# Optimization experiments

Measured on AMD Instinct MI355X. Metric: run time of the kernel, lower is better.

The kernel has to match this reference:

```python
import jax, jax.numpy as jnp
import numpy as np

NEG = -1000000.0  # mask value used by the original module


def setup_inputs() -> dict:
    key = jax.random.key(0)
    ks = jax.random.split(key, 8)
    N, D_IN, D_Q, D_K, E = 8192, 512, 512, 512, 262144
    s = 1.0 / np.sqrt(D_IN)
    return {
        "x": jax.random.normal(ks[0], (N, D_IN), dtype=jnp.float32),
        "edge_index": jax.random.randint(ks[1], (2, E), 0, N, dtype=jnp.int64),
        "Wq": jax.random.normal(ks[2], (D_IN, D_Q), dtype=jnp.float32) * s,
        "bq": jax.random.normal(ks[3], (D_Q,), dtype=jnp.float32) * 0.01,
        "Wk": jax.random.normal(ks[4], (D_IN, D_K), dtype=jnp.float32) * s,
        "bk": jax.random.normal(ks[5], (D_K,), dtype=jnp.float32) * 0.01,
        "Wv": jax.random.normal(ks[6], (D_IN, D_K), dtype=jnp.float32) * s,
        "bv": jax.random.normal(ks[7], (D_K,), dtype=jnp.float32) * 0.01,
    }


def reference(x, edge_index, Wq, bq, Wk, bk, Wv, bv):
    # Linear projections (x: [N, D_in])
    q = x @ Wq + bq  # [N, Dq]
    k = x @ Wk + bk  # [N, Dk]
    v = x @ Wv + bv  # [N, Dk]

    N = x.shape[0]
    # Dense adjacency from edge list (matches torch scatter adjacency[e0, e1] = 1)
    adj = jnp.zeros((N, N), dtype=x.dtype).at[edge_index[0], edge_index[1]].set(1.0)

    # Full scores (ptr=None branch), scaled by sqrt(Dq)
    a = (q @ k.T) / jnp.sqrt(jnp.asarray(q.shape[-1], dtype=x.dtype))
    a = a * adj + (1.0 - adj) * NEG

    attn = jax.nn.softmax(a, axis=-1)  # [N, N]
    return attn @ v  # [N, Dk]
```

## Files before the change

### kernel.cpp

```cpp
#include <hip/hip_runtime.h>


#define N_NODES 8192
#define DIM 512
#define MASK_WORDS 256
#define CAPW 512

typedef __attribute__((ext_vector_type(8))) short short8;
typedef __attribute__((ext_vector_type(4))) float f32x4;

__device__ __forceinline__ unsigned short f2bf(float f) {
    unsigned int u = __float_as_uint(f);
    u += 0x7fffu + ((u >> 16) & 1u);
    return (unsigned short)(u >> 16);
}
__device__ __forceinline__ float bf_lo(unsigned int w) { return __uint_as_float(w << 16); }
__device__ __forceinline__ float bf_hi(unsigned int w) { return __uint_as_float(w & 0xffff0000u); }

__device__ __forceinline__ float wred_sum(float s) {
    #pragma unroll
    for (int off = 1; off <= 32; off <<= 1) s += __shfl_xor(s, off, 64);
    return s;
}
__device__ __forceinline__ float wred_max(float s) {
    #pragma unroll
    for (int off = 1; off <= 32; off <<= 1) s = fmaxf(s, __shfl_xor(s, off, 64));
    return s;
}
__device__ __forceinline__ int wred_sumi(int s) {
    #pragma unroll
    for (int off = 1; off <= 32; off <<= 1) s += __shfl_xor(s, off, 64);
    return s;
}
__device__ __forceinline__ float dot8(uint4 a, uint4 b) {
    return bf_lo(a.x) * bf_lo(b.x) + bf_hi(a.x) * bf_hi(b.x)
         + bf_lo(a.y) * bf_lo(b.y) + bf_hi(a.y) * bf_hi(b.y)
         + bf_lo(a.z) * bf_lo(b.z) + bf_hi(a.z) * bf_hi(b.z)
         + bf_lo(a.w) * bf_lo(b.w) + bf_hi(a.w) * bf_hi(b.w);
}

__global__ __launch_bounds__(256) void prep(
    const float* __restrict__ x, unsigned short* __restrict__ xb,
    const float* __restrict__ Wq, const float* __restrict__ Wk,
    const float* __restrict__ Wv, unsigned short* __restrict__ Wt,
    const int* __restrict__ ei, unsigned int* __restrict__ mask, int E)
{
    __shared__ float sm[32][33];
    const int b = blockIdx.x;
    if (b < 4096) {
        int i = b * 256 + threadIdx.x;
        float4 f = ((const float4*)x)[i];
        ushort4 o;
        o.x = f2bf(f.x); o.y = f2bf(f.y); o.z = f2bf(f.z); o.w = f2bf(f.w);
        ((ushort4*)xb)[i] = o;
    } else if (b < 4864) {
        int bb = b - 4096;
        int which = bb >> 8, t = bb & 255;
        const float* __restrict__ W = (which == 0) ? Wq : (which == 1) ? Wk : Wv;
        unsigned short* __restrict__ outp = Wt + (size_t)which * DIM * DIM;
        int n0 = (t & 15) * 32, k0 = (t >> 4) * 32;
        int tx = threadIdx.x & 31, ty = threadIdx.x >> 5;
        #pragma unroll
        for (int r = 0; r < 4; ++r)
            sm[ty + 8 * r][tx] = W[(size_t)(k0 + ty + 8 * r) * DIM + n0 + tx];
        __syncthreads();
        #pragma unroll
        for (int r = 0; r < 4; ++r)
            outp[(size_t)(n0 + ty + 8 * r) * DIM + k0 + tx] = f2bf(sm[tx][ty + 8 * r]);
    } else {
        int e = (b - 4864) * 256 + threadIdx.x;
        if (e < E) {
            int src = ei[e];
            int dst = ei[E + e];
            atomicOr(&mask[(size_t)src * MASK_WORDS + (dst >> 5)], 1u << (dst & 31));
        }
    }
}

__device__ __forceinline__ void load_lds16(const unsigned short* g, unsigned short* l) {
    __builtin_amdgcn_global_load_lds(
        (const __attribute__((address_space(1))) unsigned int*)g,
        (__attribute__((address_space(3))) unsigned int*)l, 16, 0, 0);
}

__global__ __launch_bounds__(256) void mfma_gemm(
    const unsigned short* __restrict__ xb, const unsigned short* __restrict__ Wt,
    const float* __restrict__ bq, const float* __restrict__ bk, const float* __restrict__ bv,
    unsigned short* __restrict__ q, unsigned short* __restrict__ k, unsigned short* __restrict__ v)
{
    const int which = blockIdx.z;
    const unsigned short* __restrict__ Bm = Wt + (size_t)which * DIM * DIM;
    const float* __restrict__ bias = (which == 0) ? bq : (which == 1) ? bk : bv;
    unsigned short* __restrict__ outp = (which == 0) ? q : (which == 1) ? k : v;

    const int row0 = blockIdx.y * 128;
    const int col0 = blockIdx.x * 128;
    const int tid = threadIdx.x;
    const int lane = tid & 63;
    const int w = tid >> 6;
    const int wm = (w >> 1) * 64;
    const int wn = (w & 1) * 64;
    const int L = lane & 15;
    const int quad = lane >> 4;

    __shared__ unsigned short As[128 * 32];
    __shared__ unsigned short Bs[128 * 32];

    f32x4 zero = {0.f, 0.f, 0.f, 0.f};
    f32x4 acc[4][4];
    #pragma unroll
    for (int i = 0; i < 4; ++i)
        #pragma unroll
        for (int j = 0; j < 4; ++j) acc[i][j] = zero;

    const int m0 = tid >> 2;
    const int ko = (tid & 3) << 3;

    for (int k0 = 0; k0 < DIM; k0 += 32) {
        load_lds16(xb + (size_t)(row0 + m0) * DIM + k0 + ko,      As + tid * 8);
        load_lds16(xb + (size_t)(row0 + 64 + m0) * DIM + k0 + ko, As + 2048 + tid * 8);
        load_lds16(Bm + (size_t)(col0 + m0) * DIM + k0 + ko,      Bs + tid * 8);
        load_lds16(Bm + (size_t)(col0 + 64 + m0) * DIM + k0 + ko, Bs + 2048 + tid * 8);
        __syncthreads();

        short8 a[4], bfr[4];
        #pragma unroll
        for (int i = 0; i < 4; ++i)
            a[i] = *(const short8*)(const void*)&As[(wm + i * 16 + L) * 32 + quad * 8];
        #pragma unroll
        for (int j = 0; j < 4; ++j)
            bfr[j] = *(const short8*)(const void*)&Bs[(wn + j * 16 + L) * 32 + quad * 8];

        #pragma unroll
        for (int i = 0; i < 4; ++i)
            #pragma unroll
            for (int j = 0; j < 4; ++j)
                acc[i][j] = __builtin_amdgcn_mfma_f32_16x16x32_bf16(a[i], bfr[j], acc[i][j], 0, 0, 0);
        __syncthreads();
    }

    float biasv[4];
    #pragma unroll
    for (int j = 0; j < 4; ++j) biasv[j] = bias[col0 + wn + j * 16 + L];
    #pragma unroll
    for (int i = 0; i < 4; ++i) {
        int r0 = row0 + wm + i * 16 + quad * 4;
        #pragma unroll
        for (int j = 0; j < 4; ++j) {
            int c = col0 + wn + j * 16 + L;
            #pragma unroll
            for (int r = 0; r < 4; ++r)
                outp[(size_t)(r0 + r) * DIM + c] = f2bf(acc[i][j][r] + biasv[j]);
        }
    }
}

__global__ __launch_bounds__(256) void attn_kernel(
    const unsigned short* __restrict__ q, const unsigned short* __restrict__ k,
    const unsigned short* __restrict__ v, const unsigned int* __restrict__ mask,
    float* __restrict__ out)
{
    __shared__ unsigned short nbr[4][CAPW];
    __shared__ float pw[4][CAPW];
    __shared__ int cnt[4];

    const int tid = threadIdx.x;
    const int lane = tid & 63;
    const int wid = tid >> 6;
    const int row = blockIdx.x * 4 + wid;

    const uint4 qv = *(const uint4*)(q + (size_t)row * DIM + lane * 8);
    const unsigned int* __restrict__ mrow = mask + (size_t)row * MASK_WORDS;

    int pc = 0;
    #pragma unroll
    for (int t = 0; t < 4; ++t) pc += __popc(mrow[lane + 64 * t]);
    const int total = wred_sumi(pc);

    float o[8];
    #pragma unroll
    for (int i = 0; i < 8; ++i) o[i] = 0.f;

    if (total == 0) {
        for (int j = 0; j < N_NODES; ++j) {
            uint4 vv = *(const uint4*)(v + (size_t)j * DIM + lane * 8);
            o[0] += bf_lo(vv.x); o[1] += bf_hi(vv.x);
            o[2] += bf_lo(vv.y); o[3] += bf_hi(vv.y);
            o[4] += bf_lo(vv.z); o[5] += bf_hi(vv.z);
            o[6] += bf_lo(vv.w); o[7] += bf_hi(vv.w);
        }
        float4 r0 = {o[0], o[1], o[2], o[3]};
        float4 r1 = {o[4], o[5], o[6], o[7]};
        const float s = 1.0f / N_NODES;
        r0.x *= s; r0.y *= s; r0.z *= s; r0.w *= s;
        r1.x *= s; r1.y *= s; r1.z *= s; r1.w *= s;
        *(float4*)(out + (size_t)row * DIM + lane * 8) = r0;
        *(float4*)(out + (size_t)row * DIM + lane * 8 + 4) = r1;
        return;
    }

    const int nchunks = (total <= CAPW) ? 1 : 16;
    const int wpc = (nchunks == 1) ? MASK_WORDS : 16;
    const float scale = 0.044194173824159220f;

    float m_run = -3.0e38f, l_run = 0.f;

    for (int c = 0; c < nchunks; ++c) {
        if (lane == 0) cnt[wid] = 0;
        for (int wi = lane; wi < wpc; wi += 64) {
            unsigned int ww = mrow[c * wpc + wi];
            while (ww) {
                int bpos = __ffs(ww) - 1; ww &= ww - 1;
                int pos = atomicAdd(&cnt[wid], 1);
                nbr[wid][pos] = (unsigned short)((c * wpc + wi) * 32 + bpos);
            }
        }
        const int cn = cnt[wid];
        if (cn == 0) continue;

        for (int p = 0; p < cn; p += 2) {
            int j0 = nbr[wid][p];
            int j1 = nbr[wid][(p + 1 < cn) ? p + 1 : p];
            uint4 k0v = *(const uint4*)(k + (size_t)j0 * DIM + lane * 8);
            uint4 k1v = *(const uint4*)(k + (size_t)j1 * DIM + lane * 8);
            float s0 = wred_sum(dot8(qv, k0v));
            float s1 = wred_sum(dot8(qv, k1v));
            if (lane == 0) {
                pw[wid][p] = s0 * scale;
                if (p + 1 < cn) pw[wid][p + 1] = s1 * scale;
            }
        }

        float mc = -3.0e38f;
        for (int p = lane; p < cn; p += 64) mc = fmaxf(mc, pw[wid][p]);
        mc = wred_max(mc);
        const float mnew = fmaxf(m_run, mc);
        const float f = __expf(m_run - mnew);
        float ls = 0.f;
        for (int p = lane; p < cn; p += 64) {
            float e = __expf(pw[wid][p] - mnew);
            pw[wid][p] = e;
            ls += e;
        }
        l_run = l_run * f + wred_sum(ls);
        m_run = mnew;
        #pragma unroll
        for (int i = 0; i < 8; ++i) o[i] *= f;

        int p = 0;
        for (; p + 2 <= cn; p += 2) {
            int j0 = nbr[wid][p], j1 = nbr[wid][p + 1];
            float w0 = pw[wid][p], w1 = pw[wid][p + 1];
            uint4 v0 = *(const uint4*)(v + (size_t)j0 * DIM + lane * 8);
            uint4 v1 = *(const uint4*)(v + (size_t)j1 * DIM + lane * 8);
            o[0] += w0 * bf_lo(v0.x) + w1 * bf_lo(v1.x);
            o[1] += w0 * bf_hi(v0.x) + w1 * bf_hi(v1.x);
            o[2] += w0 * bf_lo(v0.y) + w1 * bf_lo(v1.y);
            o[3] += w0 * bf_hi(v0.y) + w1 * bf_hi(v1.y);
            o[4] += w0 * bf_lo(v0.z) + w1 * bf_lo(v1.z);
            o[5] += w0 * bf_hi(v0.z) + w1 * bf_hi(v1.z);
            o[6] += w0 * bf_lo(v0.w) + w1 * bf_lo(v1.w);
            o[7] += w0 * bf_hi(v0.w) + w1 * bf_hi(v1.w);
        }
        if (p < cn) {
            int j0 = nbr[wid][p];
            float w0 = pw[wid][p];
            uint4 v0 = *(const uint4*)(v + (size_t)j0 * DIM + lane * 8);
            o[0] += w0 * bf_lo(v0.x); o[1] += w0 * bf_hi(v0.x);
            o[2] += w0 * bf_lo(v0.y); o[3] += w0 * bf_hi(v0.y);
            o[4] += w0 * bf_lo(v0.z); o[5] += w0 * bf_hi(v0.z);
            o[6] += w0 * bf_lo(v0.w); o[7] += w0 * bf_hi(v0.w);
        }
    }

    const float inv = 1.0f / l_run;
    float4 r0 = {o[0] * inv, o[1] * inv, o[2] * inv, o[3] * inv};
    float4 r1 = {o[4] * inv, o[5] * inv, o[6] * inv, o[7] * inv};
    *(float4*)(out + (size_t)row * DIM + lane * 8) = r0;
    *(float4*)(out + (size_t)row * DIM + lane * 8 + 4) = r1;
}

extern "C" void kernel_launch(void* const* d_in, const int* in_sizes, int n_in,
                              void* d_out, int out_size, void* d_ws, size_t ws_size,
                              hipStream_t stream)
{
    const float* x  = (const float*)d_in[0];
    const int*   ei = (const int*)d_in[1];
    const float* Wq = (const float*)d_in[2];
    const float* bq = (const float*)d_in[3];
    const float* Wk = (const float*)d_in[4];
    const float* bk = (const float*)d_in[5];
    const float* Wv = (const float*)d_in[6];
    const float* bv = (const float*)d_in[7];
    float* out = (float*)d_out;

    const int E = in_sizes[1] / 2;
    const size_t NM = (size_t)N_NODES * DIM;

    unsigned short* xb = (unsigned short*)d_ws;
    unsigned short* Wt = xb + NM;
    unsigned short* qb = Wt + (size_t)3 * DIM * DIM;
    unsigned short* kb = qb + NM;
    unsigned short* vb = kb + NM;
    unsigned int* mask = (unsigned int*)(vb + NM);

    hipMemsetAsync(mask, 0, (size_t)N_NODES * MASK_WORDS * sizeof(unsigned int), stream);

    prep<<<4864 + (E + 255) / 256, 256, 0, stream>>>(x, xb, Wq, Wk, Wv, Wt, ei, mask, E);

    mfma_gemm<<<dim3(DIM / 128, N_NODES / 128, 3), 256, 0, stream>>>(
        xb, Wt, bq, bk, bv, qb, kb, vb);

    attn_kernel<<<N_NODES / 4, 256, 0, stream>>>(qb, kb, vb, mask, out);
}
```

Baseline: 173.1 us.

## Split each attention row across four waves, fuse mask clear, remap GEMM tiles by XCD

The attention kernel now gives each row a whole block. Each of the four waves handles a quarter of the neighbour mask, keeps its own online softmax, and the partial results are merged through LDS, with gathers unrolled by four. The mask memset moves into the bf16 conversion kernel and the edge scatter becomes its own launch. GEMM tiles are remapped so row blocks group per XCD for L2 locality. This aims to shorten per-row serial latency and improve occupancy, at the cost of extra block syncs, LDS traffic and one more launch.

```diff
diff --git a/kernel.cpp b/kernel.cpp
--- a/kernel.cpp
+++ b/kernel.cpp
@@ -4,7 +4,7 @@
 #define N_NODES 8192
 #define DIM 512
 #define MASK_WORDS 256
-#define CAPW 512
+#define SCAP 256
 
 typedef __attribute__((ext_vector_type(8))) short short8;
 typedef __attribute__((ext_vector_type(4))) float f32x4;
@@ -39,11 +39,11 @@
          + bf_lo(a.w) * bf_lo(b.w) + bf_hi(a.w) * bf_hi(b.w);
 }
 
-__global__ __launch_bounds__(256) void prep(
+__global__ __launch_bounds__(256) void prep1(
     const float* __restrict__ x, unsigned short* __restrict__ xb,
     const float* __restrict__ Wq, const float* __restrict__ Wk,
     const float* __restrict__ Wv, unsigned short* __restrict__ Wt,
-    const int* __restrict__ ei, unsigned int* __restrict__ mask, int E)
+    unsigned int* __restrict__ mask)
 {
     __shared__ float sm[32][33];
     const int b = blockIdx.x;
@@ -53,7 +53,8 @@
         ushort4 o;
         o.x = f2bf(f.x); o.y = f2bf(f.y); o.z = f2bf(f.z); o.w = f2bf(f.w);
         ((ushort4*)xb)[i] = o;
-    } else if (b < 4864) {
+        ((uint2*)mask)[i] = make_uint2(0u, 0u);
+    } else {
         int bb = b - 4096;
         int which = bb >> 8, t = bb & 255;
         const float* __restrict__ W = (which == 0) ? Wq : (which == 1) ? Wk : Wv;
@@ -67,14 +68,17 @@
         #pragma unroll
         for (int r = 0; r < 4; ++r)
             outp[(size_t)(n0 + ty + 8 * r) * DIM + k0 + tx] = f2bf(sm[tx][ty + 8 * r]);
-    } else {
-        int e = (b - 4864) * 256 + threadIdx.x;
-        if (e < E) {
-            int src = ei[e];
-            int dst = ei[E + e];
-            atomicOr(&mask[(size_t)src * MASK_WORDS + (dst >> 5)], 1u << (dst & 31));
-        }
-    }
+    }
+}
+
+__global__ __launch_bounds__(256) void prep2(
+    const int* __restrict__ ei, unsigned int* __restrict__ mask, int E)
+{
+    int e = blockIdx.x * 256 + threadIdx.x;
+    if (e >= E) return;
+    int src = ei[e];
+    int dst = ei[E + e];
+    atomicOr(&mask[(size_t)src * MASK_WORDS + (dst >> 5)], 1u << (dst & 31));
 }
 
 __device__ __forceinline__ void load_lds16(const unsigned short* g, unsigned short* l) {
@@ -86,15 +90,21 @@
 __global__ __launch_bounds__(256) void mfma_gemm(
     const unsigned short* __restrict__ xb, const unsigned short* __restrict__ Wt,
     const float* __restrict__ bq, const float* __restrict__ bk, const float* __restrict__ bv,
-    unsigned short* __restrict__ q, unsigned short* __restrict__ k, unsigned short* __restrict__ v)
-{
-    const int which = blockIdx.z;
+    unsigned short* __restrict__ qkv)
+{
+    const int p = blockIdx.x;
+    const int xcd = p & 7;
+    const int s = p >> 3;
+    const int mloc = s / 12;
+    const int n = s - 12 * mloc;
+    const int which = n >> 2;
+    const int row0 = (xcd * 8 + mloc) << 7;
+    const int col0 = (n & 3) << 7;
+
     const unsigned short* __restrict__ Bm = Wt + (size_t)which * DIM * DIM;
     const float* __restrict__ bias = (which == 0) ? bq : (which == 1) ? bk : bv;
-    unsigned short* __restrict__ outp = (which == 0) ? q : (which == 1) ? k : v;
-
-    const int row0 = blockIdx.y * 128;
-    const int col0 = blockIdx.x * 128;
+    unsigned short* __restrict__ outp = qkv + (size_t)which * N_NODES * DIM;
+
     const int tid = threadIdx.x;
     const int lane = tid & 63;
     const int w = tid >> 6;
@@ -160,74 +170,85 @@
     const unsigned short* __restrict__ v, const unsigned int* __restrict__ mask,
     float* __restrict__ out)
 {
-    __shared__ unsigned short nbr[4][CAPW];
-    __shared__ float pw[4][CAPW];
+    __shared__ unsigned short nbr[4][SCAP];
+    __shared__ float pw[4][SCAP];
+    __shared__ float buf[4][DIM];
+    __shared__ float sm_m[4], sm_l[4];
+    __shared__ int degs[4];
     __shared__ int cnt[4];
 
     const int tid = threadIdx.x;
     const int lane = tid & 63;
     const int wid = tid >> 6;
-    const int row = blockIdx.x * 4 + wid;
+    const int row = blockIdx.x;
 
     const uint4 qv = *(const uint4*)(q + (size_t)row * DIM + lane * 8);
-    const unsigned int* __restrict__ mrow = mask + (size_t)row * MASK_WORDS;
-
-    int pc = 0;
-    #pragma unroll
-    for (int t = 0; t < 4; ++t) pc += __popc(mrow[lane + 64 * t]);
-    const int total = wred_sumi(pc);
+    const unsigned int mw = mask[(size_t)row * MASK_WORDS + wid * 64 + lane];
+
+    const int pc_s = wred_sumi(__popc(mw));
+    if (lane == 0) degs[wid] = pc_s;
+    __syncthreads();
+    const int total = degs[0] + degs[1] + degs[2] + degs[3];
 
     float o[8];
     #pragma unroll
     for (int i = 0; i < 8; ++i) o[i] = 0.f;
 
     if (total == 0) {
-        for (int j = 0; j < N_NODES; ++j) {
+        for (int j = wid * 2048; j < (wid + 1) * 2048; ++j) {
             uint4 vv = *(const uint4*)(v + (size_t)j * DIM + lane * 8);
             o[0] += bf_lo(vv.x); o[1] += bf_hi(vv.x);
             o[2] += bf_lo(vv.y); o[3] += bf_hi(vv.y);
             o[4] += bf_lo(vv.z); o[5] += bf_hi(vv.z);
             o[6] += bf_lo(vv.w); o[7] += bf_hi(vv.w);
         }
-        float4 r0 = {o[0], o[1], o[2], o[3]};
-        float4 r1 = {o[4], o[5], o[6], o[7]};
-        const float s = 1.0f / N_NODES;
-        r0.x *= s; r0.y *= s; r0.z *= s; r0.w *= s;
-        r1.x *= s; r1.y *= s; r1.z *= s; r1.w *= s;
-        *(float4*)(out + (size_t)row * DIM + lane * 8) = r0;
-        *(float4*)(out + (size_t)row * DIM + lane * 8 + 4) = r1;
+        #pragma unroll
+        for (int i = 0; i < 8; ++i) buf[wid][lane * 8 + i] = o[i];
+        __syncthreads();
+        const float sc = 1.0f / N_NODES;
+        int c = tid * 2;
+        float2 r;
+        r.x = (buf[0][c] + buf[1][c] + buf[2][c] + buf[3][c]) * sc;
+        r.y = (buf[0][c + 1] + buf[1][c + 1] + buf[2][c + 1] + buf[3][c + 1]) * sc;
+        *(float2*)(out + (size_t)row * DIM + c) = r;
         return;
     }
 
-    const int nchunks = (total <= CAPW) ? 1 : 16;
-    const int wpc = (nchunks == 1) ? MASK_WORDS : 16;
     const float scale = 0.044194173824159220f;
-
     float m_run = -3.0e38f, l_run = 0.f;
 
+    const int nchunks = (pc_s <= SCAP) ? 1 : 8;
     for (int c = 0; c < nchunks; ++c) {
         if (lane == 0) cnt[wid] = 0;
-        for (int wi = lane; wi < wpc; wi += 64) {
-            unsigned int ww = mrow[c * wpc + wi];
+        if (nchunks == 1 || (lane >> 3) == c) {
+            unsigned int ww = mw;
             while (ww) {
                 int bpos = __ffs(ww) - 1; ww &= ww - 1;
                 int pos = atomicAdd(&cnt[wid], 1);
-                nbr[wid][pos] = (unsigned short)((c * wpc + wi) * 32 + bpos);
+                nbr[wid][pos] = (unsigned short)((wid * 64 + lane) * 32 + bpos);
             }
         }
         const int cn = cnt[wid];
         if (cn == 0) continue;
 
-        for (int p = 0; p < cn; p += 2) {
-            int j0 = nbr[wid][p];
-            int j1 = nbr[wid][(p + 1 < cn) ? p + 1 : p];
+        for (int p0 = 0; p0 < cn; p0 += 4) {
+            int j0 = nbr[wid][p0];
+            int j1 = nbr[wid][(p0 + 1 < cn) ? p0 + 1 : p0];
+            int j2 = nbr[wid][(p0 + 2 < cn) ? p0 + 2 : p0];
+            int j3 = nbr[wid][(p0 + 3 < cn) ? p0 + 3 : p0];
             uint4 k0v = *(const uint4*)(k + (size_t)j0 * DIM + lane * 8);
             uint4 k1v = *(const uint4*)(k + (size_t)j1 * DIM + lane * 8);
+            uint4 k2v = *(const uint4*)(k + (size_t)j2 * DIM + lane * 8);
+            uint4 k3v = *(const uint4*)(k + (size_t)j3 * DIM + lane * 8);
             float s0 = wred_sum(dot8(qv, k0v));
             float s1 = wred_sum(dot8(qv, k1v));
+            float s2 = wred_sum(dot8(qv, k2v));
+            float s3 = wred_sum(dot8(qv, k3v));
             if (lane == 0) {
-                pw[wid][p] = s0 * scale;
-                if (p + 1 < cn) pw[wid][p + 1] = s1 * scale;
+                pw[wid][p0] = s0 * scale;
+                if (p0 + 1 < cn) pw[wid][p0 + 1] = s1 * scale;
+                if (p0 + 2 < cn) pw[wid][p0 + 2] = s2 * scale;
+                if (p0 + 3 < cn) pw[wid][p0 + 3] = s3 * scale;
             }
         }
 
@@ -247,37 +268,46 @@
         #pragma unroll
         for (int i = 0; i < 8; ++i) o[i] *= f;
 
-        int p = 0;
-        for (; p + 2 <= cn; p += 2) {
-            int j0 = nbr[wid][p], j1 = nbr[wid][p + 1];
-            float w0 = pw[wid][p], w1 = pw[wid][p + 1];
+        for (int p0 = 0; p0 < cn; p0 += 4) {
+            int j0 = nbr[wid][p0];
+            int j1 = nbr[wid][(p0 + 1 < cn) ? p0 + 1 : p0];
+            int j2 = nbr[wid][(p0 + 2 < cn) ? p0 + 2 : p0];
+            int j3 = nbr[wid][(p0 + 3 < cn) ? p0 + 3 : p0];
+            float w0 = pw[wid][p0];
+            float w1 = (p0 + 1 < cn) ? pw[wid][p0 + 1] : 0.f;
+            float w2 = (p0 + 2 < cn) ? pw[wid][p0 + 2] : 0.f;
+            float w3 = (p0 + 3 < cn) ? pw[wid][p0 + 3] : 0.f;
             uint4 v0 = *(const uint4*)(v + (size_t)j0 * DIM + lane * 8);
             uint4 v1 = *(const uint4*)(v + (size_t)j1 * DIM + lane * 8);
-            o[0] += w0 * bf_lo(v0.x) + w1 * bf_lo(v1.x);
-            o[1] += w0 * bf_hi(v0.x) + w1 * bf_hi(v1.x);
-            o[2] += w0 * bf_lo(v0.y) + w1 * bf_lo(v1.y);
-            o[3] += w0 * bf_hi(v0.y) + w1 * bf_hi(v1.y);
-            o[4] += w0 * bf_lo(v0.z) + w1 * bf_lo(v1.z);
-            o[5] += w0 * bf_hi(v0.z) + w1 * bf_hi(v1.z);
-            o[6] += w0 * bf_lo(v0.w) + w1 * bf_lo(v1.w);
-            o[7] += w0 * bf_hi(v0.w) + w1 * bf_hi(v1.w);
-        }
-        if (p < cn) {
-            int j0 = nbr[wid][p];
-            float w0 = pw[wid][p];
-            uint4 v0 = *(const uint4*)(v + (size_t)j0 * DIM + lane * 8);
-            o[0] += w0 * bf_lo(v0.x); o[1] += w0 * bf_hi(v0.x);
-            o[2] += w0 * bf_lo(v0.y); o[3] += w0 * bf_hi(v0.y);
-            o[4] += w0 * bf_lo(v0.z); o[5] += w0 * bf_hi(v0.z);
-            o[6] += w0 * bf_lo(v0.w); o[7] += w0 * bf_hi(v0.w);
-        }
-    }
-
-    const float inv = 1.0f / l_run;
-    float4 r0 = {o[0] * inv, o[1] * inv, o[2] * inv, o[3] * inv};
-    float4 r1 = {o[4] * inv, o[5] * inv, o[6] * inv, o[7] * inv};
-    *(float4*)(out + (size_t)row * DIM + lane * 8) = r0;
-    *(float4*)(out + (size_t)row * DIM + lane * 8 + 4) = r1;
+            uint4 v2 = *(const uint4*)(v + (size_t)j2 * DIM + lane * 8);
+            uint4 v3 = *(const uint4*)(v + (size_t)j3 * DIM + lane * 8);
+            o[0] += w0 * bf_lo(v0.x) + w1 * bf_lo(v1.x) + w2 * bf_lo(v2.x) + w3 * bf_lo(v3.x);
+            o[1] += w0 * bf_hi(v0.x) + w1 * bf_hi(v1.x) + w2 * bf_hi(v2.x) + w3 * bf_hi(v3.x);
+            o[2] += w0 * bf_lo(v0.y) + w1 * bf_lo(v1.y) + w2 * bf_lo(v2.y) + w3 * bf_lo(v3.y);
+            o[3] += w0 * bf_hi(v0.y) + w1 * bf_hi(v1.y) + w2 * bf_hi(v2.y) + w3 * bf_hi(v3.y);
+            o[4] += w0 * bf_lo(v0.z) + w1 * bf_lo(v1.z) + w2 * bf_lo(v2.z) + w3 * bf_lo(v3.z);
+            o[5] += w0 * bf_hi(v0.z) + w1 * bf_hi(v1.z) + w2 * bf_hi(v2.z) + w3 * bf_hi(v3.z);
+            o[6] += w0 * bf_lo(v0.w) + w1 * bf_lo(v1.w) + w2 * bf_lo(v2.w) + w3 * bf_lo(v3.w);
+            o[7] += w0 * bf_hi(v0.w) + w1 * bf_hi(v1.w) + w2 * bf_hi(v2.w) + w3 * bf_hi(v3.w);
+        }
+    }
+
+    if (lane == 0) { sm_m[wid] = m_run; sm_l[wid] = l_run; }
+    __syncthreads();
+    const float M = fmaxf(fmaxf(sm_m[0], sm_m[1]), fmaxf(sm_m[2], sm_m[3]));
+    const float Lsum = sm_l[0] * __expf(sm_m[0] - M) + sm_l[1] * __expf(sm_m[1] - M)
+                     + sm_l[2] * __expf(sm_m[2] - M) + sm_l[3] * __expf(sm_m[3] - M);
+    const float r = __expf(m_run - M);
+    #pragma unroll
+    for (int i = 0; i < 8; ++i) buf[wid][lane * 8 + i] = o[i] * r;
+    __syncthreads();
+
+    const float inv = 1.0f / Lsum;
+    int c = tid * 2;
+    float2 res;
+    res.x = (buf[0][c] + buf[1][c] + buf[2][c] + buf[3][c]) * inv;
+    res.y = (buf[0][c + 1] + buf[1][c + 1] + buf[2][c + 1] + buf[3][c + 1]) * inv;
+    *(float2*)(out + (size_t)row * DIM + c) = res;
 }
 
 extern "C" void kernel_launch(void* const* d_in, const int* in_sizes, int n_in,
@@ -299,17 +329,16 @@
 
     unsigned short* xb = (unsigned short*)d_ws;
     unsigned short* Wt = xb + NM;
-    unsigned short* qb = Wt + (size_t)3 * DIM * DIM;
-    unsigned short* kb = qb + NM;
-    unsigned short* vb = kb + NM;
-    unsigned int* mask = (unsigned int*)(vb + NM);
-
-    hipMemsetAsync(mask, 0, (size_t)N_NODES * MASK_WORDS * sizeof(unsigned int), stream);
-
-    prep<<<4864 + (E + 255) / 256, 256, 0, stream>>>(x, xb, Wq, Wk, Wv, Wt, ei, mask, E);
-
-    mfma_gemm<<<dim3(DIM / 128, N_NODES / 128, 3), 256, 0, stream>>>(
-        xb, Wt, bq, bk, bv, qb, kb, vb);
-
-    attn_kernel<<<N_NODES / 4, 256, 0, stream>>>(qb, kb, vb, mask, out);
-}
+    unsigned short* qkv = Wt + (size_t)3 * DIM * DIM;
+    unsigned short* qb = qkv;
+    unsigned short* kb = qkv + NM;
+    unsigned short* vb = qkv + 2 * NM;
+    unsigned int* mask = (unsigned int*)(qkv + 3 * NM);
+
+    prep1<<<4864, 256, 0, stream>>>(x, xb, Wq, Wk, Wv, Wt, mask);
+    prep2<<<(E + 255) / 256, 256, 0, stream>>>(ei, mask, E);
+
+    mfma_gemm<<<768, 256, 0, stream>>>(xb, Wt, bq, bk, bv, qkv);
+
+    attn_kernel<<<N_NODES, 256, 0, stream>>>(qb, kb, vb, mask, out);
+}
```

Result: slower. 180.6 us (+4.3%).
